# Kernel optimization log

Hardware: AMD Instinct MI355X
Metric: run time of the kernel (lower is better)

## Reference

```python
import jax, jax.numpy as jnp
import numpy as np
import math

N_HEADS = 16

def alibi_slopes(n_heads: int) -> jnp.ndarray:
    # n_heads=16 is a power of two, so the simple geometric series applies.
    ratio = 2.0 ** (-8.0 / n_heads)
    slopes = ratio ** np.arange(1, n_heads + 1, dtype=np.float64)
    return jnp.asarray(slopes, dtype=jnp.float32).reshape(1, n_heads, 1, 1)

def setup_inputs() -> dict:
    key = jax.random.key(0)
    kq, kk, kv = jax.random.split(key, 3)
    B, H, S, D = 2, N_HEADS, 2048, 64
    return {
        "query": jax.random.normal(kq, (B, H, S, D), dtype=jnp.float32),
        "key": jax.random.normal(kk, (B, H, S, D), dtype=jnp.float32),
        "value": jax.random.normal(kv, (B, H, S, D), dtype=jnp.float32),
        "attention_mask": jnp.ones((B, S), dtype=bool),
    }

def reference(query, key, value, attention_mask):
    B, H, Q, D = query.shape
    K = key.shape[2]
    scale = 1.0 / math.sqrt(D)
    # (B,H,Q,K) attention logits
    scores = jnp.einsum("bhqd,bhkd->bhqk", query, key) * scale
    # ALiBi causal biases: distances arange(1-K, 1), shape (1,1,1,K), times per-head slopes
    distances = jnp.arange(1 - K, 1, dtype=jnp.float32).reshape(1, 1, 1, K)
    scores = scores + distances * alibi_slopes(H)
    # merge padding mask (B,1,1,K) with causal tril mask (1,1,Q,K)
    causal = jnp.tril(jnp.ones((K, K), dtype=bool))[K - Q:K, :K][None, None]
    mask = attention_mask[:, None, None, :] & causal
    blocked = jnp.finfo(scores.dtype).min
    scores = jnp.where(mask, scores, blocked)
    probs = jax.nn.softmax(scores, axis=-1)
    return jnp.einsum("bhqk,bhkd->bhqd", probs, value)
```

## Files before the change

### kernel.cpp

```cpp
#include <hip/hip_runtime.h>
#include <stdint.h>

#define S 2048
#define D 64
#define BH 32
#define SD (S*D)
#define LDK 72
#define KSCALE 0.1803368801111244f

typedef __attribute__((ext_vector_type(4))) short s16x4;
typedef __attribute__((ext_vector_type(8))) short s16x8;
typedef __attribute__((ext_vector_type(4))) float fx4;

__device__ __forceinline__ float fast_exp2(float x) { return __builtin_amdgcn_exp2f(x); }

__device__ __forceinline__ short f2bf(float f) {
  uint32_t u = __builtin_bit_cast(uint32_t, f);
  u += 0x7fffu + ((u >> 16) & 1u);
  return (short)(u >> 16);
}

__device__ __forceinline__ uint32_t cvt_pk_bf16(float a, float b) {
  uint32_t r;
  asm("v_cvt_pk_bf16_f32 %0, %1, %2" : "=v"(r) : "v"(a), "v"(b));
  return r;
}

__device__ __forceinline__ void async_cp16(const short* g, short* lds) {
  __builtin_amdgcn_global_load_lds((const __attribute__((address_space(1))) void*)g,
                                   (__attribute__((address_space(3))) void*)lds, 16, 0, 0);
}

__global__ __launch_bounds__(256) void prep_kv(const float* __restrict__ K,
                                               const float* __restrict__ V,
                                               short* __restrict__ kb,
                                               short* __restrict__ vtb) {
  const int kt = blockIdx.x;
  const int bh = blockIdx.y;
  const int tid = threadIdx.x;
  __shared__ float tile[64][65];

  const float* kp = K + (size_t)bh*SD + (size_t)kt*64*D;
  short* kd = kb + (size_t)bh*SD + (size_t)kt*64*D;
  #pragma unroll
  for (int i = 0; i < 4; i++) {
    int f4 = i*256 + tid;
    float4 f = ((const float4*)kp)[f4];
    s16x4 hh;
    hh[0]=f2bf(f.x*KSCALE); hh[1]=f2bf(f.y*KSCALE);
    hh[2]=f2bf(f.z*KSCALE); hh[3]=f2bf(f.w*KSCALE);
    ((s16x4*)kd)[f4] = hh;
  }

  const float* vp = V + (size_t)bh*SD + (size_t)kt*64*D;
  #pragma unroll
  for (int i = 0; i < 4; i++) {
    int row = i*16 + (tid >> 4);
    int c4 = tid & 15;
    float4 f = ((const float4*)(vp + row*D))[c4];
    tile[row][c4*4+0] = f.x; tile[row][c4*4+1] = f.y;
    tile[row][c4*4+2] = f.z; tile[row][c4*4+3] = f.w;
  }
  __syncthreads();
  int d  = tid >> 2;
  int kq = (tid & 3) * 16;
  short* vd = vtb + ((size_t)bh*32 + kt)*4096 + d*64 + kq;
  s16x8 h0, h1;
  #pragma unroll
  for (int j = 0; j < 8; j++) h0[j] = f2bf(tile[kq+j][d]);
  #pragma unroll
  for (int j = 0; j < 8; j++) h1[j] = f2bf(tile[kq+8+j][d]);
  ((s16x8*)vd)[0] = h0;
  ((s16x8*)vd)[1] = h1;
}

__global__ __launch_bounds__(256, 4) void fattn(const float* __restrict__ Q,
                                                const short* __restrict__ Kb,
                                                const short* __restrict__ Vtb,
                                                float* __restrict__ O) {
  const int bh = blockIdx.x;
  const int qb = 31 - (int)blockIdx.y;
  const int h  = bh & 15;
  const int tid = threadIdx.x;
  const int w = tid >> 6, lane = tid & 63, quad = lane >> 4, l15 = lane & 15;
  const int q0 = qb * 64;

  __shared__ __align__(16) short kbuf[2][64*64];
  __shared__ __align__(16) short vbuf[64*64];
  __shared__ __align__(16) short pbuf[64*LDK];
  __shared__ float lsums[4][64];

  const float LOG2E = 1.44269504f;
  const float slope2 = fast_exp2(-0.5f*(float)(h+1)) * LOG2E;

  float cq[4];
  #pragma unroll
  for (int qt = 0; qt < 4; qt++)
    cq[qt] = slope2 * (float)(q0 + qt*16 + l15) + 8.0f*LOG2E;
  float koff[4];
  #pragma unroll
  for (int r = 0; r < 4; r++) koff[r] = slope2 * (float)(w*16 + quad*4 + r);

  s16x8 qf[4][2];
  #pragma unroll
  for (int qt = 0; qt < 4; qt++) {
    const float* qp = Q + (size_t)bh*SD + (size_t)(q0 + qt*16 + l15)*D + quad*8;
    #pragma unroll
    for (int s = 0; s < 2; s++) {
      float4 a = *(const float4*)(qp + s*32);
      float4 b = *(const float4*)(qp + s*32 + 4);
      s16x8 t;
      t[0]=f2bf(a.x); t[1]=f2bf(a.y); t[2]=f2bf(a.z); t[3]=f2bf(a.w);
      t[4]=f2bf(b.x); t[5]=f2bf(b.y); t[6]=f2bf(b.z); t[7]=f2bf(b.w);
      qf[qt][s] = t;
    }
  }

  fx4 acc[4];
  #pragma unroll
  for (int nt = 0; nt < 4; nt++) acc[nt] = (fx4){0.f,0.f,0.f,0.f};
  float lsum[4] = {0.f,0.f,0.f,0.f};

  const short* kg = Kb  + (size_t)bh*SD;
  const short* vg = Vtb + (size_t)bh*SD;

  int soff[2];
  #pragma unroll
  for (int i = 0; i < 2; i++) {
    int cl  = w*128 + i*64 + lane;
    int row = cl >> 3, cc = cl & 7;
    soff[i] = row*64 + ((cc ^ (row & 7)) << 3);
  }
  const int ldst = (w*128 + lane) * 8;
  const int swz  = l15 & 7;

  async_cp16(kg + soff[0], &kbuf[0][ldst]);
  async_cp16(kg + soff[1], &kbuf[0][ldst + 512]);

  for (int kt = 0; kt <= qb; kt++) {
    __syncthreads();

    const short* vT = vg + (size_t)kt*4096;
    async_cp16(vT + soff[0], vbuf + ldst);
    async_cp16(vT + soff[1], vbuf + ldst + 512);
    const bool more = (kt < qb);
    if (more) {
      const short* kT = kg + (size_t)(kt+1)*4096;
      short* kn = &kbuf[(kt+1)&1][0];
      async_cp16(kT + soff[0], kn + ldst);
      async_cp16(kT + soff[1], kn + ldst + 512);
    }
    const short* kc = &kbuf[kt&1][0];

    const int kbase = kt*64;
    const float ckb = slope2 * (float)kbase;
    float ecq[4];
    #pragma unroll
    for (int qt = 0; qt < 4; qt++) ecq[qt] = ckb - cq[qt];
    fx4 sc[4];
    #pragma unroll
    for (int qt = 0; qt < 4; qt++)
      #pragma unroll
      for (int r = 0; r < 4; r++) sc[qt][r] = koff[r] + ecq[qt];

    #pragma unroll
    for (int s = 0; s < 2; s++) {
      s16x8 kf = *(const s16x8*)&kc[(w*16 + l15)*64 + (((s*4 + quad) ^ swz) << 3)];
      #pragma unroll
      for (int qt = 0; qt < 4; qt++)
        sc[qt] = __builtin_amdgcn_mfma_f32_16x16x32_bf16(kf, qf[qt][s], sc[qt], 0, 0, 0);
    }

    if (kt < qb) {
      #pragma unroll
      for (int qt = 0; qt < 4; qt++) {
        float p0 = fast_exp2(sc[qt][0]);
        float p1 = fast_exp2(sc[qt][1]);
        float p2 = fast_exp2(sc[qt][2]);
        float p3 = fast_exp2(sc[qt][3]);
        uint32_t w0 = cvt_pk_bf16(p0, p1);
        uint32_t w1 = cvt_pk_bf16(p2, p3);
        lsum[qt] += __builtin_bit_cast(float, w0 << 16) + __builtin_bit_cast(float, w0 & 0xffff0000u)
                  + __builtin_bit_cast(float, w1 << 16) + __builtin_bit_cast(float, w1 & 0xffff0000u);
        *(uint2*)&pbuf[(qt*16 + l15)*LDK + w*16 + quad*4] = (uint2){w0, w1};
      }
    } else {
      const int kl = w*16 + quad*4;
      #pragma unroll
      for (int qt = 0; qt < 4; qt++) {
        const int ql = qt*16 + l15;
        float p[4];
        #pragma unroll
        for (int r = 0; r < 4; r++)
          p[r] = (kl + r <= ql) ? fast_exp2(sc[qt][r]) : 0.f;
        uint32_t w0 = cvt_pk_bf16(p[0], p[1]);
        uint32_t w1 = cvt_pk_bf16(p[2], p[3]);
        lsum[qt] += __builtin_bit_cast(float, w0 << 16) + __builtin_bit_cast(float, w0 & 0xffff0000u)
                  + __builtin_bit_cast(float, w1 << 16) + __builtin_bit_cast(float, w1 & 0xffff0000u);
        *(uint2*)&pbuf[(qt*16 + l15)*LDK + w*16 + quad*4] = (uint2){w0, w1};
      }
    }

    __builtin_amdgcn_sched_barrier(0);
    asm volatile("s_waitcnt lgkmcnt(0)" ::: "memory");
    __builtin_amdgcn_s_barrier();
    __builtin_amdgcn_sched_barrier(0);

    if (more) __builtin_amdgcn_s_waitcnt(0x0F72);
    else      __builtin_amdgcn_s_waitcnt(0x0F70);

    #pragma unroll
    for (int s = 0; s < 2; s++) {
      s16x8 pf = *(const s16x8*)&pbuf[(w*16 + l15)*LDK + s*32 + quad*8];
      #pragma unroll
      for (int nt = 0; nt < 4; nt++) {
        s16x8 vf = *(const s16x8*)&vbuf[(nt*16 + l15)*64 + (((s*4 + quad) ^ swz) << 3)];
        acc[nt] = __builtin_amdgcn_mfma_f32_16x16x32_bf16(pf, vf, acc[nt], 0, 0, 0);
      }
    }
  }

  #pragma unroll
  for (int qt = 0; qt < 4; qt++) {
    lsum[qt] += __shfl_xor(lsum[qt], 16, 64);
    lsum[qt] += __shfl_xor(lsum[qt], 32, 64);
  }
  if (quad == 0) {
    #pragma unroll
    for (int qt = 0; qt < 4; qt++) lsums[w][qt*16 + l15] = lsum[qt];
  }
  __syncthreads();

  float inv[4];
  #pragma unroll
  for (int r = 0; r < 4; r++) {
    const int qrow = w*16 + quad*4 + r;
    inv[r] = 1.0f / (lsums[0][qrow] + lsums[1][qrow] + lsums[2][qrow] + lsums[3][qrow]);
  }

  float* op = O + (size_t)bh*SD;
  #pragma unroll
  for (int nt = 0; nt < 4; nt++)
    #pragma unroll
    for (int r = 0; r < 4; r++)
      op[(size_t)(q0 + w*16 + quad*4 + r)*D + nt*16 + l15] = acc[nt][r] * inv[r];
}

extern "C" void kernel_launch(void* const* d_in, const int* in_sizes, int n_in,
                              void* d_out, int out_size, void* d_ws, size_t ws_size,
                              hipStream_t stream) {
  const float* Q = (const float*)d_in[0];
  const float* K = (const float*)d_in[1];
  const float* V = (const float*)d_in[2];
  float* O = (float*)d_out;
  short* kb  = (short*)d_ws;
  short* vtb = kb + (size_t)BH*SD;
  prep_kv<<<dim3(32, 32), 256, 0, stream>>>(K, V, kb, vtb);
  fattn<<<dim3(32, 32), 256, 0, stream>>>(Q, kb, vtb, O);
}
```

Baseline: 127.0 us.

## Software-pipeline PV matmul one tile behind with double-buffered V and P

Moves the P·V MFMA for tile kt-1 into iteration kt, ahead of the QK^T MFMA, and double-buffers the V and P shared-memory tiles. This removes the second barrier and explicit waitcnt inside each iteration, so the V load for the current tile overlaps with a full iteration of work. The last tile's PV runs after the loop behind one extra sync. The larger LDS footprint forces the launch bound down from 4 to 3 blocks per CU, which lowers occupancy.

```diff
diff --git a/kernel.cpp b/kernel.cpp
--- a/kernel.cpp
+++ b/kernel.cpp
@@ -74,7 +74,7 @@
   ((s16x8*)vd)[1] = h1;
 }
 
-__global__ __launch_bounds__(256, 4) void fattn(const float* __restrict__ Q,
+__global__ __launch_bounds__(256, 3) void fattn(const float* __restrict__ Q,
                                                 const short* __restrict__ Kb,
                                                 const short* __restrict__ Vtb,
                                                 float* __restrict__ O) {
@@ -86,8 +86,8 @@
   const int q0 = qb * 64;
 
   __shared__ __align__(16) short kbuf[2][64*64];
-  __shared__ __align__(16) short vbuf[64*64];
-  __shared__ __align__(16) short pbuf[64*LDK];
+  __shared__ __align__(16) short vbuf[2][64*64];
+  __shared__ __align__(16) short pbuf[2][64*LDK];
   __shared__ float lsums[4][64];
 
   const float LOG2E = 1.44269504f;
@@ -134,6 +134,18 @@
   const int ldst = (w*128 + lane) * 8;
   const int swz  = l15 & 7;
 
+  auto do_pv = [&](int p) {
+    #pragma unroll
+    for (int s = 0; s < 2; s++) {
+      s16x8 pf = *(const s16x8*)&pbuf[p][(w*16 + l15)*LDK + s*32 + quad*8];
+      #pragma unroll
+      for (int nt = 0; nt < 4; nt++) {
+        s16x8 vf = *(const s16x8*)&vbuf[p][(nt*16 + l15)*64 + (((s*4 + quad) ^ swz) << 3)];
+        acc[nt] = __builtin_amdgcn_mfma_f32_16x16x32_bf16(pf, vf, acc[nt], 0, 0, 0);
+      }
+    }
+  };
+
   async_cp16(kg + soff[0], &kbuf[0][ldst]);
   async_cp16(kg + soff[1], &kbuf[0][ldst + 512]);
 
@@ -141,16 +153,16 @@
     __syncthreads();
 
     const short* vT = vg + (size_t)kt*4096;
-    async_cp16(vT + soff[0], vbuf + ldst);
-    async_cp16(vT + soff[1], vbuf + ldst + 512);
-    const bool more = (kt < qb);
-    if (more) {
+    async_cp16(vT + soff[0], &vbuf[kt&1][ldst]);
+    async_cp16(vT + soff[1], &vbuf[kt&1][ldst + 512]);
+    if (kt < qb) {
       const short* kT = kg + (size_t)(kt+1)*4096;
       short* kn = &kbuf[(kt+1)&1][0];
       async_cp16(kT + soff[0], kn + ldst);
       async_cp16(kT + soff[1], kn + ldst + 512);
     }
-    const short* kc = &kbuf[kt&1][0];
+
+    if (kt > 0) do_pv((kt-1)&1);
 
     const int kbase = kt*64;
     const float ckb = slope2 * (float)kbase;
@@ -163,6 +175,7 @@
       #pragma unroll
       for (int r = 0; r < 4; r++) sc[qt][r] = koff[r] + ecq[qt];
 
+    const short* kc = &kbuf[kt&1][0];
     #pragma unroll
     for (int s = 0; s < 2; s++) {
       s16x8 kf = *(const s16x8*)&kc[(w*16 + l15)*64 + (((s*4 + quad) ^ swz) << 3)];
@@ -171,6 +184,7 @@
         sc[qt] = __builtin_amdgcn_mfma_f32_16x16x32_bf16(kf, qf[qt][s], sc[qt], 0, 0, 0);
     }
 
+    short* pw = &pbuf[kt&1][0];
     if (kt < qb) {
       #pragma unroll
       for (int qt = 0; qt < 4; qt++) {
@@ -182,7 +196,7 @@
         uint32_t w1 = cvt_pk_bf16(p2, p3);
         lsum[qt] += __builtin_bit_cast(float, w0 << 16) + __builtin_bit_cast(float, w0 & 0xffff0000u)
                   + __builtin_bit_cast(float, w1 << 16) + __builtin_bit_cast(float, w1 & 0xffff0000u);
-        *(uint2*)&pbuf[(qt*16 + l15)*LDK + w*16 + quad*4] = (uint2){w0, w1};
+        *(uint2*)&pw[(qt*16 + l15)*LDK + w*16 + quad*4] = (uint2){w0, w1};
       }
     } else {
       const int kl = w*16 + quad*4;
@@ -197,28 +211,13 @@
         uint32_t w1 = cvt_pk_bf16(p[2], p[3]);
         lsum[qt] += __builtin_bit_cast(float, w0 << 16) + __builtin_bit_cast(float, w0 & 0xffff0000u)
                   + __builtin_bit_cast(float, w1 << 16) + __builtin_bit_cast(float, w1 & 0xffff0000u);
-        *(uint2*)&pbuf[(qt*16 + l15)*LDK + w*16 + quad*4] = (uint2){w0, w1};
+        *(uint2*)&pw[(qt*16 + l15)*LDK + w*16 + quad*4] = (uint2){w0, w1};
       }
     }
-
-    __builtin_amdgcn_sched_barrier(0);
-    asm volatile("s_waitcnt lgkmcnt(0)" ::: "memory");
-    __builtin_amdgcn_s_barrier();
-    __builtin_amdgcn_sched_barrier(0);
-
-    if (more) __builtin_amdgcn_s_waitcnt(0x0F72);
-    else      __builtin_amdgcn_s_waitcnt(0x0F70);
-
-    #pragma unroll
-    for (int s = 0; s < 2; s++) {
-      s16x8 pf = *(const s16x8*)&pbuf[(w*16 + l15)*LDK + s*32 + quad*8];
-      #pragma unroll
-      for (int nt = 0; nt < 4; nt++) {
-        s16x8 vf = *(const s16x8*)&vbuf[(nt*16 + l15)*64 + (((s*4 + quad) ^ swz) << 3)];
-        acc[nt] = __builtin_amdgcn_mfma_f32_16x16x32_bf16(pf, vf, acc[nt], 0, 0, 0);
-      }
-    }
-  }
+  }
+
+  __syncthreads();
+  do_pv(qb & 1);
 
   #pragma unroll
   for (int qt = 0; qt < 4; qt++) {
```

New measurement: 130.7 us. +3.0%, slower.
